# Performance work log

Hardware: AMD Instinct MI355X
Metric: run time of the kernel (lower is better)

The kernel has to match this reference:

```python
import jax, jax.numpy as jnp
import numpy as np

D_MODEL = 1024
NHEAD = 16
D_HEAD = D_MODEL // NHEAD
D_FF = 4096
B, S = 2, 2048
EPS = 1e-5


def _linear_params(key, d_in, d_out):
    kw, kb = jax.random.split(key)
    bound = 1.0 / np.sqrt(d_in)
    W = jax.random.uniform(kw, (d_out, d_in), jnp.float32, -bound, bound)
    b = jax.random.uniform(kb, (d_out,), jnp.float32, -bound, bound)
    return W, b


def setup_inputs() -> dict:
    key = jax.random.key(0)
    ks = jax.random.split(key, 8)
    x = jax.random.normal(ks[0], (B, S, D_MODEL), jnp.float32)
    Wq, bq = _linear_params(ks[1], D_MODEL, D_MODEL)
    Wk, bk = _linear_params(ks[2], D_MODEL, D_MODEL)
    Wv, bv = _linear_params(ks[3], D_MODEL, D_MODEL)
    Wo, bo = _linear_params(ks[4], D_MODEL, D_MODEL)
    W1, b1 = _linear_params(ks[5], D_MODEL, D_FF)
    W2, b2 = _linear_params(ks[6], D_FF, D_MODEL)
    g1 = jnp.ones((D_MODEL,), jnp.float32); be1 = jnp.zeros((D_MODEL,), jnp.float32)
    g2 = jnp.ones((D_MODEL,), jnp.float32); be2 = jnp.zeros((D_MODEL,), jnp.float32)
    return dict(x=x, Wq=Wq, bq=bq, Wk=Wk, bk=bk, Wv=Wv, bv=bv, Wo=Wo, bo=bo,
                W1=W1, b1=b1, W2=W2, b2=b2, g1=g1, be1=be1, g2=g2, be2=be2)


def _layernorm(x, g, b):
    mu = jnp.mean(x, axis=-1, keepdims=True)
    var = jnp.mean(jnp.square(x - mu), axis=-1, keepdims=True)
    return (x - mu) * jax.lax.rsqrt(var + EPS) * g + b


def reference(x, Wq, bq, Wk, bk, Wv, bv, Wo, bo, W1, b1, W2, b2, g1, be1, g2, be2):
    b_, s_, _ = x.shape
    # QKV projections (nn.Linear: x @ W.T + b)
    q = x @ Wq.T + bq
    k = x @ Wk.T + bk
    v = x @ Wv.T + bv
    # split heads -> [b, h, s, d_head]
    qh = q.reshape(b_, s_, NHEAD, D_HEAD).transpose(0, 2, 1, 3)
    kh = k.reshape(b_, s_, NHEAD, D_HEAD).transpose(0, 2, 1, 3)
    vh = v.reshape(b_, s_, NHEAD, D_HEAD).transpose(0, 2, 1, 3)
    scores = jnp.einsum('bhqd,bhkd->bhqk', qh, kh) / jnp.sqrt(jnp.float32(D_HEAD))
    attn_w = jax.nn.softmax(scores, axis=-1)
    attn_out = jnp.einsum('bhqk,bhkd->bhqd', attn_w, vh)
    attn_concat = attn_out.transpose(0, 2, 1, 3).reshape(b_, s_, D_MODEL)
    attn_proj = attn_concat @ Wo.T + bo
    # residual + LN1
    h = _layernorm(x + attn_proj, g1, be1)
    # FFN
    ffn = jax.nn.relu(h @ W1.T + b1) @ W2.T + b2
    # residual + LN2
    return _layernorm(h + ffn, g2, be2)
```

## Files before the change

### kernel.cpp

```cpp
#include <hip/hip_runtime.h>
#include <hip/hip_bf16.h>

#define D_MODEL 1024
#define NHEAD 16
#define D_HEAD 64
#define D_FF 4096
#define BATCH 2
#define SEQ 2048
#define M_TOK (BATCH * SEQ)
#define EPS 1e-5f
#define QKV_N 3072

using bf16 = __hip_bfloat16;
typedef __attribute__((ext_vector_type(8))) short short8;
typedef __attribute__((ext_vector_type(4))) short short4v;
typedef __attribute__((ext_vector_type(4))) float float4v;
typedef __attribute__((ext_vector_type(16))) float float16v;

__device__ __forceinline__ float b2f(unsigned short u) {
    union { unsigned int i; float f; } v; v.i = ((unsigned int)u) << 16; return v.f;
}
__device__ __forceinline__ unsigned short f2b(float f) {
    union { float f; unsigned int u; } v; v.f = f;
    unsigned int r = v.u + 0x7FFFu + ((v.u >> 16) & 1u);
    return (unsigned short)(r >> 16);
}
__device__ __forceinline__ float loadAt(const void* p, size_t i, int f32) {
    if (f32) return ((const float*)p)[i];
    return b2f(((const unsigned short*)p)[i]);
}
__device__ __forceinline__ void async16(const void* g, void* lds) {
    __builtin_amdgcn_global_load_lds(
        (const __attribute__((address_space(1))) unsigned int*)g,
        (__attribute__((address_space(3))) unsigned int*)lds, 16, 0, 0);
}

__global__ void detect_kernel(const unsigned short* __restrict__ x, int* __restrict__ flag) {
    __shared__ int cnt;
    if (threadIdx.x == 0) cnt = 0;
    __syncthreads();
    int c = 0;
    for (int i = threadIdx.x; i < 8192; i += 256) {
        unsigned short u = x[i];
        int e = (u >> 7) & 0xFF;
        if (e >= 0xF0) c++;
    }
    atomicAdd(&cnt, c);
    __syncthreads();
    if (threadIdx.x == 0) { flag[0] = (cnt > 16) ? 1 : 0; flag[1] = 0; }
}

__global__ __launch_bounds__(256) void cast_bf16_kernel(
    const void* __restrict__ src, bf16* __restrict__ dst, int n,
    const int* __restrict__ flagp) {
    const int f32 = *flagp;
    int i0 = (blockIdx.x * 256 + threadIdx.x) * 8;
    if (i0 >= n) return;
    short8 v;
    if (f32) {
        const float* pf = (const float*)src + i0;
        float4v f0 = *(const float4v*)pf;
        float4v f1 = *(const float4v*)(pf + 4);
#pragma unroll
        for (int i = 0; i < 4; i++) { v[i] = (short)f2b(f0[i]); v[4 + i] = (short)f2b(f1[i]); }
    } else {
        v = *(const short8*)((const short*)src + i0);
    }
    *(short8*)((short*)dst + i0) = v;
}

__global__ __launch_bounds__(256) void cast3_bf16_kernel(
    const void* __restrict__ s0, const void* __restrict__ s1,
    const void* __restrict__ s2, bf16* __restrict__ dst,
    const int* __restrict__ flagp) {
    const int f32 = *flagp;
    int i0 = (blockIdx.x * 256 + threadIdx.x) * 8;
    const int part = i0 >> 20;
    const int off = i0 & ((1 << 20) - 1);
    const void* src = (part == 0) ? s0 : (part == 1) ? s1 : s2;
    short8 v;
    if (f32) {
        const float* pf = (const float*)src + off;
        float4v f0 = *(const float4v*)pf;
        float4v f1 = *(const float4v*)(pf + 4);
#pragma unroll
        for (int i = 0; i < 4; i++) { v[i] = (short)f2b(f0[i]); v[4 + i] = (short)f2b(f1[i]); }
    } else {
        v = *(const short8*)((const short*)src + off);
    }
    *(short8*)((short*)dst + i0) = v;
}

__global__ __launch_bounds__(256) void cast2_bf16_kernel(
    const void* __restrict__ s0, const void* __restrict__ s1,
    bf16* __restrict__ d0, bf16* __restrict__ d1,
    const int* __restrict__ flagp) {
    const int f32 = *flagp;
    int i0 = (blockIdx.x * 256 + threadIdx.x) * 8;
    const void* src; short* dst; int off;
    if (i0 < (1 << 20)) { src = s0; dst = (short*)d0; off = i0; }
    else                { src = s1; dst = (short*)d1; off = i0 - (1 << 20); }
    short8 v;
    if (f32) {
        const float* pf = (const float*)src + off;
        float4v f0 = *(const float4v*)pf;
        float4v f1 = *(const float4v*)(pf + 4);
#pragma unroll
        for (int i = 0; i < 4; i++) { v[i] = (short)f2b(f0[i]); v[4 + i] = (short)f2b(f1[i]); }
    } else {
        v = *(const short8*)((const short*)src + off);
    }
    *(short8*)(dst + off) = v;
}

__device__ __forceinline__ void stage8(const void* src, size_t off, int f32, short* dst) {
    short8 v;
    if (f32) {
        const float* pf = (const float*)src + off;
        float4v f0 = *(const float4v*)pf;
        float4v f1 = *(const float4v*)(pf + 4);
#pragma unroll
        for (int i = 0; i < 4; i++) { v[i] = (short)f2b(f0[i]); v[4 + i] = (short)f2b(f1[i]); }
    } else {
        v = *(const short8*)((const short*)src + off);
    }
    *(short8*)dst = v;
}

template <int MF, int NF, bool RELU, bool BDYN>
__global__ __launch_bounds__(256) void gemm_mfma(
    const bf16* __restrict__ A, const void* __restrict__ B,
    const void* __restrict__ bias0, const void* __restrict__ bias1,
    const void* __restrict__ bias2, int nb1, int nb2,
    bf16* __restrict__ C, int N, int K, const int* __restrict__ inFlagp) {
    constexpr int BM = 32 * MF, BN = 32 * NF;
    __shared__ short As[BM * 64];
    __shared__ short Bs[BN * 64];
    const int tid = threadIdx.x;
    const int lane = tid & 63;
    const int wv = tid >> 6;
    const int wm = wv & 1, wn = wv >> 1;
    const int quad = lane >> 4, lrow = lane & 15;
    const int rowM = blockIdx.y * BM;
    const int rowN = blockIdx.x * BN;
    const int inf = *inFlagp;

    float4v acc[MF][NF];
    const float4v zero = {0.f, 0.f, 0.f, 0.f};
#pragma unroll
    for (int i = 0; i < MF; i++)
#pragma unroll
        for (int j = 0; j < NF; j++) acc[i][j] = zero;

    const int sRow = lane >> 3;
    const int gChunk = (lane & 7) ^ sRow;

    for (int k0 = 0; k0 < K; k0 += 64) {
#pragma unroll
        for (int rd = 0; rd < MF; rd++) {
            const short* gp = (const short*)A +
                (size_t)(rowM + rd * 32 + wv * 8 + sRow) * K + k0 + gChunk * 8;
            async16(gp, &As[rd * 2048 + wv * 512]);
        }
        if (!BDYN) {
#pragma unroll
            for (int rd = 0; rd < NF; rd++) {
                const short* gp = (const short*)B +
                    (size_t)(rowN + rd * 32 + wv * 8 + sRow) * K + k0 + gChunk * 8;
                async16(gp, &Bs[rd * 2048 + wv * 512]);
            }
        } else {
            const int brow = tid >> 2;
            const int c0 = (tid & 3) * 2;
#pragma unroll
            for (int cc = 0; cc < 2; cc++) {
                int slot = c0 + cc;
                int g = slot ^ (brow & 7);
                stage8(B, (size_t)(rowN + brow) * K + k0 + g * 8, inf,
                       &Bs[brow * 64 + slot * 8]);
            }
        }
        __syncthreads();
#pragma unroll
        for (int ks = 0; ks < 2; ks++) {
            short8 a_frag[MF], b_frag[NF];
#pragma unroll
            for (int i = 0; i < MF; i++) {
                const int row = wm * MF * 16 + i * 16 + lrow;
                const int slot = (ks * 4 + quad) ^ (row & 7);
                a_frag[i] = *(const short8*)&As[row * 64 + slot * 8];
            }
#pragma unroll
            for (int j = 0; j < NF; j++) {
                const int row = wn * NF * 16 + j * 16 + lrow;
                const int slot = (ks * 4 + quad) ^ (row & 7);
                b_frag[j] = *(const short8*)&Bs[row * 64 + slot * 8];
            }
#pragma unroll
            for (int i = 0; i < MF; i++)
#pragma unroll
                for (int j = 0; j < NF; j++)
                    acc[i][j] = __builtin_amdgcn_mfma_f32_16x16x32_bf16(
                        a_frag[i], b_frag[j], acc[i][j], 0, 0, 0);
        }
        __syncthreads();
    }

    const int mB = rowM + wm * MF * 16, nB = rowN + wn * NF * 16;
    unsigned short* Cu = (unsigned short*)C;
#pragma unroll
    for (int j = 0; j < NF; j++) {
        const int col = nB + j * 16 + lrow;
        float bv;
        if (col < nb1)      bv = loadAt(bias0, col, inf);
        else if (col < nb2) bv = loadAt(bias1, col - nb1, inf);
        else                bv = loadAt(bias2, col - nb2, inf);
#pragma unroll
        for (int i = 0; i < MF; i++) {
#pragma unroll
            for (int r = 0; r < 4; r++) {
                const int rowg = mB + i * 16 + quad * 4 + r;
                float vv = acc[i][j][r] + bv;
                if (RELU) vv = fmaxf(vv, 0.0f);
                Cu[(size_t)rowg * N + col] = f2b(vv);
            }
        }
    }
}

#define FSTRIDE 66
__global__ __launch_bounds__(256) void flash_attn_kernel(
    const bf16* __restrict__ Qb, const bf16* __restrict__ Kb,
    const bf16* __restrict__ Vb, bf16* __restrict__ O) {
    const int bid = blockIdx.x;
    const int qt = bid & 15;
    const int h  = (bid >> 4) & 15;
    const int b  = bid >> 8;
    const int q0 = qt * 128;
    const int tid = threadIdx.x;
    const int lane = tid & 63;
    const int wv = tid >> 6;
    const int half = lane >> 5;
    const int l31 = lane & 31;

    __shared__ short Ps[128 * FSTRIDE];
    __shared__ short Ks[64 * 64];
    __shared__ short Vt[64 * FSTRIDE];

    const size_t headOff = (size_t)h * D_HEAD;
    const float SCF = 0.18033688f;

    {
        int r = tid >> 1, c0 = (tid & 1) * 32;
        const short* src = (const short*)Qb + (size_t)(b * SEQ + q0 + r) * QKV_N + headOff + c0;
#pragma unroll
        for (int ch = 0; ch < 4; ch++) {
            short8 v = *(const short8*)(src + ch * 8);
            short8 o;
#pragma unroll
            for (int e = 0; e < 8; e++)
                o[e] = (short)f2b(b2f((unsigned short)v[e]) * SCF);
            *(short8*)&Ps[r * FSTRIDE + c0 + ch * 8] = o;
        }
    }
    __syncthreads();
    short8 a_q[4];
#pragma unroll
    for (int ks = 0; ks < 4; ks++)
        a_q[ks] = *(const short8*)&Ps[(wv * 32 + l31) * FSTRIDE + ks * 16 + half * 8];

    float16v o_acc[2];
    float lsum[16];
#pragma unroll
    for (int i = 0; i < 16; i++) { o_acc[0][i] = 0.f; o_acc[1][i] = 0.f; lsum[i] = 0.f; }

    const int sRow = lane >> 3;
    const int gChunk = (lane & 7) ^ sRow;

    for (int j0 = 0; j0 < SEQ; j0 += 64) {
        __syncthreads();
#pragma unroll
        for (int rd = 0; rd < 2; rd++) {
            const short* gp = (const short*)Kb +
                (size_t)(b * SEQ + j0 + wv * 16 + rd * 8 + sRow) * QKV_N + headOff + gChunk * 8;
            async16(gp, &Ks[(wv * 16 + rd * 8) * 64]);
        }
        {
            int jp = (tid & 31) * 2, d0 = (tid >> 5) * 8;
            const short* s0 = (const short*)Vb + (size_t)(b * SEQ + j0 + jp) * QKV_N + headOff + d0;
            short8 v0 = *(const short8*)s0;
            short8 v1 = *(const short8*)(s0 + QKV_N);
#pragma unroll
            for (int e = 0; e < 8; e++) {
                unsigned int w = (unsigned int)(unsigned short)v0[e] |
                                 ((unsigned int)(unsigned short)v1[e] << 16);
                *(unsigned int*)&Vt[(d0 + e) * FSTRIDE + jp] = w;
            }
        }
        __syncthreads();

        float16v s_acc[2];
#pragma unroll
        for (int i = 0; i < 16; i++) { s_acc[0][i] = 0.f; s_acc[1][i] = 0.f; }
#pragma unroll
        for (int ks = 0; ks < 4; ks++)
#pragma unroll
            for (int jb = 0; jb < 2; jb++) {
                const int row = jb * 32 + l31;
                const int slot = (ks * 2 + half) ^ (l31 & 7);
                short8 bfr = *(const short8*)&Ks[row * 64 + slot * 8];
                s_acc[jb] = __builtin_amdgcn_mfma_f32_32x32x16_bf16(a_q[ks], bfr, s_acc[jb], 0, 0, 0);
            }

#pragma unroll
        for (int jb = 0; jb < 2; jb++)
#pragma unroll
            for (int reg = 0; reg < 16; reg++) {
                float pv = exp2f(s_acc[jb][reg]);
                lsum[reg] += pv;
                union { float f; unsigned int u; } uu; uu.f = pv;
                const int rowC = (reg & 3) + 8 * (reg >> 2) + 4 * half;
                Ps[(wv * 32 + rowC) * FSTRIDE + jb * 32 + l31] = (short)(uu.u >> 16);
            }

#pragma unroll
        for (int ks = 0; ks < 4; ks++) {
            short8 pa = *(const short8*)&Ps[(wv * 32 + l31) * FSTRIDE + ks * 16 + half * 8];
#pragma unroll
            for (int db = 0; db < 2; db++) {
                short8 vb = *(const short8*)&Vt[(db * 32 + l31) * FSTRIDE + ks * 16 + half * 8];
                o_acc[db] = __builtin_amdgcn_mfma_f32_32x32x16_bf16(pa, vb, o_acc[db], 0, 0, 0);
            }
        }
    }

    float invl[16];
#pragma unroll
    for (int reg = 0; reg < 16; reg++) {
        float t = lsum[reg];
        t += __shfl_xor(t, 1);
        t += __shfl_xor(t, 2);
        t += __shfl_xor(t, 4);
        t += __shfl_xor(t, 8);
        t += __shfl_xor(t, 16);
        invl[reg] = 1.0f / t;
    }
    unsigned short* Ou = (unsigned short*)O;
#pragma unroll
    for (int db = 0; db < 2; db++)
#pragma unroll
        for (int reg = 0; reg < 16; reg++) {
            const int rowC = (reg & 3) + 8 * (reg >> 2) + 4 * half;
            const int rowg = b * SEQ + q0 + wv * 32 + rowC;
            Ou[(size_t)rowg * D_MODEL + headOff + db * 32 + l31] =
                f2b(o_acc[db][reg] * invl[reg]);
        }
}

template <bool OUT_F32>
__global__ __launch_bounds__(256) void add_ln_kernel(
    const void* __restrict__ X, const bf16* __restrict__ R,
    const void* __restrict__ g, const void* __restrict__ be,
    void* __restrict__ Y,
    const int* __restrict__ xFlagp, const int* __restrict__ wFlagp) {
    const int xf = *xFlagp;
    const int wf = *wFlagp;
    const int row = blockIdx.x;
    const size_t base = (size_t)row * D_MODEL;
    const int tid = threadIdx.x;
    const int i0 = tid * 4;
    __shared__ float red[256];
    float v[4];
    if (xf) {
        float4v xv = *(const float4v*)((const float*)X + base + i0);
        short4v rv = *(const short4v*)((const short*)R + base + i0);
#pragma unroll
        for (int i = 0; i < 4; i++) v[i] = xv[i] + b2f((unsigned short)rv[i]);
    } else {
        short4v xv = *(const short4v*)((const short*)X + base + i0);
        short4v rv = *(const short4v*)((const short*)R + base + i0);
#pragma unroll
        for (int i = 0; i < 4; i++) v[i] = b2f((unsigned short)xv[i]) + b2f((unsigned short)rv[i]);
    }
    float s = v[0] + v[1] + v[2] + v[3];
    red[tid] = s; __syncthreads();
    for (int s2 = 128; s2 > 0; s2 >>= 1) {
        if (tid < s2) red[tid] += red[tid + s2];
        __syncthreads();
    }
    float mu = red[0] * (1.0f / D_MODEL);
    __syncthreads();
    float s2v = 0.f;
#pragma unroll
    for (int i = 0; i < 4; i++) { float dd = v[i] - mu; s2v += dd * dd; }
    red[tid] = s2v; __syncthreads();
    for (int s2 = 128; s2 > 0; s2 >>= 1) {
        if (tid < s2) red[tid] += red[tid + s2];
        __syncthreads();
    }
    float rstd = rsqrtf(red[0] * (1.0f / D_MODEL) + EPS);
    float gv[4], bv[4];
    if (wf) {
        float4v gg = *(const float4v*)((const float*)g + i0);
        float4v bb = *(const float4v*)((const float*)be + i0);
#pragma unroll
        for (int i = 0; i < 4; i++) { gv[i] = gg[i]; bv[i] = bb[i]; }
    } else {
        short4v gg = *(const short4v*)((const short*)g + i0);
        short4v bb = *(const short4v*)((const short*)be + i0);
#pragma unroll
        for (int i = 0; i < 4; i++) { gv[i] = b2f((unsigned short)gg[i]); bv[i] = b2f((unsigned short)bb[i]); }
    }
    if (OUT_F32) {
        float4v o;
#pragma unroll
        for (int i = 0; i < 4; i++) o[i] = (v[i] - mu) * rstd * gv[i] + bv[i];
        *(float4v*)((float*)Y + base + i0) = o;
    } else {
        short4v o;
#pragma unroll
        for (int i = 0; i < 4; i++) o[i] = (short)f2b((v[i] - mu) * rstd * gv[i] + bv[i]);
        *(short4v*)((short*)Y + base + i0) = o;
    }
}

extern "C" void kernel_launch(void* const* d_in, const int* in_sizes, int n_in,
                              void* d_out, int out_size, void* d_ws, size_t ws_size,
                              hipStream_t stream) {
    const void* x  = d_in[0];
    const void* Wq = d_in[1];  const void* bq = d_in[2];
    const void* Wk = d_in[3];  const void* bk = d_in[4];
    const void* Wv = d_in[5];  const void* bv = d_in[6];
    const void* Wo = d_in[7];  const void* bo = d_in[8];
    const void* W1 = d_in[9];  const void* b1 = d_in[10];
    const void* W2 = d_in[11]; const void* b2 = d_in[12];
    const void* g1 = d_in[13]; const void* be1 = d_in[14];
    const void* g2 = d_in[15]; const void* be2 = d_in[16];

    char* ws = (char*)d_ws;
    const size_t MB = 1024 * 1024;
    bf16* xb     = (bf16*)(ws + 0 * MB);
    bf16* wqkvb  = (bf16*)(ws + 8 * MB);
    bf16* wob    = (bf16*)(ws + 14 * MB);
    bf16* qkv    = (bf16*)(ws + 16 * MB);
    bf16* concat = (bf16*)(ws + 40 * MB);
    bf16* w1b    = (bf16*)(ws + 0 * MB);
    bf16* proj   = (bf16*)(ws + 16 * MB);
    bf16* hb     = (bf16*)(ws + 8 * MB);
    bf16* ffn1   = (bf16*)(ws + 16 * MB);
    bf16* ffn2   = (bf16*)(ws + 0 * MB);
    const bool castW2 = (ws_size >= 56 * MB + 8);
    bf16* w2b    = (bf16*)(ws + 48 * MB);
    int*  flag   = (int*)(ws + (castW2 ? 56 * MB : 48 * MB));

    const int* fIn = flag;
    const int* fBf = flag + 1;

    dim3 blk(256);

    detect_kernel<<<dim3(1), blk, 0, stream>>>((const unsigned short*)x, flag);
    cast_bf16_kernel<<<dim3((M_TOK * D_MODEL / 8 + 255) / 256), blk, 0, stream>>>(x, xb, M_TOK * D_MODEL, fIn);
    cast3_bf16_kernel<<<dim3(3 * D_MODEL * D_MODEL / 8 / 256), blk, 0, stream>>>(Wq, Wk, Wv, wqkvb, fIn);
    if (castW2)
        cast_bf16_kernel<<<dim3((D_FF * D_MODEL / 8 + 255) / 256), blk, 0, stream>>>(W2, w2b, D_FF * D_MODEL, fIn);
    gemm_mfma<4, 4, false, false><<<dim3(QKV_N / 128, M_TOK / 128), blk, 0, stream>>>(
        xb, wqkvb, bq, bk, bv, 1024, 2048, qkv, QKV_N, D_MODEL, fIn);
    cast2_bf16_kernel<<<dim3(5 * D_MODEL * D_MODEL / 8 / 256), blk, 0, stream>>>(Wo, W1, wob, w1b, fIn);
    flash_attn_kernel<<<dim3(BATCH * NHEAD * (SEQ / 128)), blk, 0, stream>>>(
        qkv, qkv + D_MODEL, qkv + 2 * D_MODEL, concat);
    gemm_mfma<2, 2, false, false><<<dim3(D_MODEL / 64, M_TOK / 64), blk, 0, stream>>>(
        concat, wob, bo, bo, bo, D_MODEL, D_MODEL, proj, D_MODEL, D_MODEL, fIn);
    add_ln_kernel<false><<<dim3(M_TOK), blk, 0, stream>>>(x, proj, g1, be1, hb, fIn, fIn);
    gemm_mfma<4, 4, true, false><<<dim3(D_FF / 128, M_TOK / 128), blk, 0, stream>>>(
        hb, w1b, b1, b1, b1, D_FF, D_FF, ffn1, D_FF, D_MODEL, fIn);
    if (castW2)
        gemm_mfma<2, 2, false, false><<<dim3(D_MODEL / 64, M_TOK / 64), blk, 0, stream>>>(
            ffn1, w2b, b2, b2, b2, D_MODEL, D_MODEL, ffn2, D_MODEL, D_FF, fIn);
    else
        gemm_mfma<2, 2, false, true><<<dim3(D_MODEL / 64, M_TOK / 64), blk, 0, stream>>>(
            ffn1, W2, b2, b2, b2, D_MODEL, D_MODEL, ffn2, D_MODEL, D_FF, fIn);
    add_ln_kernel<true><<<dim3(M_TOK), blk, 0, stream>>>(hb, ffn2, g2, be2, d_out, fBf, fIn);
}
```

Baseline: 405.1 us.

## Split attention key range across two blocks and merge partial outputs

The flash attention grid gains a second dimension that splits the 2048-key loop into two halves. Each half writes an unnormalized bf16 partial output and its fp32 row sums, and a new merge kernel adds the two partials and normalizes them. This doubles the number of attention blocks so more CUs stay busy, since the old grid of 512 blocks left the device underoccupied. The cost is an extra kernel launch, extra global traffic for the partials, and bf16 rounding of the unnormalized partial outputs. Workspace buffers are reassigned so the partials fit.

```diff
diff --git a/kernel.cpp b/kernel.cpp
--- a/kernel.cpp
+++ b/kernel.cpp
@@ -231,8 +231,10 @@
 #define FSTRIDE 66
 __global__ __launch_bounds__(256) void flash_attn_kernel(
     const bf16* __restrict__ Qb, const bf16* __restrict__ Kb,
-    const bf16* __restrict__ Vb, bf16* __restrict__ O) {
+    const bf16* __restrict__ Vb, bf16* __restrict__ Opart,
+    float* __restrict__ lpart) {
     const int bid = blockIdx.x;
+    const int jh  = blockIdx.y;
     const int qt = bid & 15;
     const int h  = (bid >> 4) & 15;
     const int b  = bid >> 8;
@@ -277,7 +279,8 @@
     const int sRow = lane >> 3;
     const int gChunk = (lane & 7) ^ sRow;
 
-    for (int j0 = 0; j0 < SEQ; j0 += 64) {
+    const int jBeg = jh * (SEQ / 2), jEnd = jBeg + SEQ / 2;
+    for (int j0 = jBeg; j0 < jEnd; j0 += 64) {
         __syncthreads();
 #pragma unroll
         for (int rd = 0; rd < 2; rd++) {
@@ -334,7 +337,7 @@
         }
     }
 
-    float invl[16];
+    float lred[16];
 #pragma unroll
     for (int reg = 0; reg < 16; reg++) {
         float t = lsum[reg];
@@ -343,18 +346,39 @@
         t += __shfl_xor(t, 4);
         t += __shfl_xor(t, 8);
         t += __shfl_xor(t, 16);
-        invl[reg] = 1.0f / t;
-    }
-    unsigned short* Ou = (unsigned short*)O;
-#pragma unroll
-    for (int db = 0; db < 2; db++)
-#pragma unroll
-        for (int reg = 0; reg < 16; reg++) {
-            const int rowC = (reg & 3) + 8 * (reg >> 2) + 4 * half;
-            const int rowg = b * SEQ + q0 + wv * 32 + rowC;
-            Ou[(size_t)rowg * D_MODEL + headOff + db * 32 + l31] =
-                f2b(o_acc[db][reg] * invl[reg]);
-        }
+        lred[reg] = t;
+    }
+    unsigned short* Ou = (unsigned short*)Opart + (size_t)jh * M_TOK * D_MODEL;
+    float* lp = lpart + (size_t)jh * M_TOK * NHEAD;
+#pragma unroll
+    for (int reg = 0; reg < 16; reg++) {
+        const int rowC = (reg & 3) + 8 * (reg >> 2) + 4 * half;
+        const int rowg = b * SEQ + q0 + wv * 32 + rowC;
+#pragma unroll
+        for (int db = 0; db < 2; db++)
+            Ou[(size_t)rowg * D_MODEL + headOff + db * 32 + l31] = f2b(o_acc[db][reg]);
+        if (l31 == 0) lp[rowg * NHEAD + h] = lred[reg];
+    }
+}
+
+__global__ __launch_bounds__(256) void merge_kernel(
+    const bf16* __restrict__ Opart, const float* __restrict__ lpart,
+    bf16* __restrict__ O) {
+    const int gid = blockIdx.x * 256 + threadIdx.x;
+    const size_t i0 = (size_t)gid * 8;
+    const int rowg = (int)(i0 >> 10);
+    const int hd = (int)(i0 & 1023);
+    const int h = hd >> 6;
+    short8 o0 = *(const short8*)((const short*)Opart + i0);
+    short8 o1 = *(const short8*)((const short*)Opart + (size_t)M_TOK * D_MODEL + i0);
+    float l0 = lpart[rowg * NHEAD + h];
+    float l1 = lpart[M_TOK * NHEAD + rowg * NHEAD + h];
+    float inv = 1.0f / (l0 + l1);
+    short8 o;
+#pragma unroll
+    for (int e = 0; e < 8; e++)
+        o[e] = (short)f2b((b2f((unsigned short)o0[e]) + b2f((unsigned short)o1[e])) * inv);
+    *(short8*)((short*)O + i0) = o;
 }
 
 template <bool OUT_F32>
@@ -441,11 +465,13 @@
     const size_t MB = 1024 * 1024;
     bf16* xb     = (bf16*)(ws + 0 * MB);
     bf16* wqkvb  = (bf16*)(ws + 8 * MB);
-    bf16* wob    = (bf16*)(ws + 14 * MB);
     bf16* qkv    = (bf16*)(ws + 16 * MB);
-    bf16* concat = (bf16*)(ws + 40 * MB);
+    bf16* opart  = (bf16*)(ws + 0 * MB);
+    float* lpart = (float*)(ws + 40 * MB);
+    bf16* concat = (bf16*)(ws + 16 * MB);
     bf16* w1b    = (bf16*)(ws + 0 * MB);
-    bf16* proj   = (bf16*)(ws + 16 * MB);
+    bf16* wob    = (bf16*)(ws + 32 * MB);
+    bf16* proj   = (bf16*)(ws + 24 * MB);
     bf16* hb     = (bf16*)(ws + 8 * MB);
     bf16* ffn1   = (bf16*)(ws + 16 * MB);
     bf16* ffn2   = (bf16*)(ws + 0 * MB);
@@ -465,9 +491,10 @@
         cast_bf16_kernel<<<dim3((D_FF * D_MODEL / 8 + 255) / 256), blk, 0, stream>>>(W2, w2b, D_FF * D_MODEL, fIn);
     gemm_mfma<4, 4, false, false><<<dim3(QKV_N / 128, M_TOK / 128), blk, 0, stream>>>(
         xb, wqkvb, bq, bk, bv, 1024, 2048, qkv, QKV_N, D_MODEL, fIn);
+    flash_attn_kernel<<<dim3(BATCH * NHEAD * (SEQ / 128), 2), blk, 0, stream>>>(
+        qkv, qkv + D_MODEL, qkv + 2 * D_MODEL, opart, lpart);
+    merge_kernel<<<dim3(M_TOK * D_MODEL / 8 / 256), blk, 0, stream>>>(opart, lpart, concat);
     cast2_bf16_kernel<<<dim3(5 * D_MODEL * D_MODEL / 8 / 256), blk, 0, stream>>>(Wo, W1, wob, w1b, fIn);
-    flash_attn_kernel<<<dim3(BATCH * NHEAD * (SEQ / 128)), blk, 0, stream>>>(
-        qkv, qkv + D_MODEL, qkv + 2 * D_MODEL, concat);
     gemm_mfma<2, 2, false, false><<<dim3(D_MODEL / 64, M_TOK / 64), blk, 0, stream>>>(
         concat, wob, bo, bo, bo, D_MODEL, D_MODEL, proj, D_MODEL, D_MODEL, fIn);
     add_ln_kernel<false><<<dim3(M_TOK), blk, 0, stream>>>(x, proj, g1, be1, hb, fIn, fIn);
```

After: 395.7 us. 2.3% less time.
